# Kernel tuning notes

Measured on AMD Instinct MI355X. Metric: run time of the kernel, lower is better.

## Reference

```python
import jax, jax.numpy as jnp
import numpy as np

B, T, C = 4, 2048, 1024
N_HEAD = 16
HS = C // N_HEAD  # head_size = 64


def setup_inputs() -> dict:
    key = jax.random.key(0)
    k1, k2, k3 = jax.random.split(key, 3)
    x = jax.random.normal(k1, (B, T, C), dtype=jnp.float32)
    # torch Linear(in, out, bias=False); stored here as (in, out) so y = x @ W
    W_attn = jax.random.normal(k2, (C, 3 * C), dtype=jnp.float32) * (C ** -0.5)
    W_proj = jax.random.normal(k3, (C, C), dtype=jnp.float32) * (C ** -0.5)
    return {"x": x, "W_attn": W_attn, "W_proj": W_proj}


def reference(x, W_attn, W_proj):
    Bq, Tq, Cq = x.shape
    qkv = x @ W_attn                              # (B, T, 3C)
    q, k, v = jnp.split(qkv, 3, axis=-1)          # each (B, T, C)
    # (B, T, C) -> (B, H, T, hs)
    q = q.reshape(Bq, Tq, N_HEAD, HS).transpose(0, 2, 1, 3)
    k = k.reshape(Bq, Tq, N_HEAD, HS).transpose(0, 2, 1, 3)
    v = v.reshape(Bq, Tq, N_HEAD, HS).transpose(0, 2, 1, 3)
    scale = HS ** -0.5
    att = jnp.einsum("bhqd,bhkd->bhqk", q, k) * scale  # (B, H, T, T)
    causal = jnp.tril(jnp.ones((Tq, Tq), dtype=bool))
    att = jnp.where(causal[None, None], att, jnp.finfo(att.dtype).min)
    att = jax.nn.softmax(att, axis=-1)
    y = jnp.einsum("bhqk,bhkd->bhqd", att, v)     # (B, H, T, hs)
    y = y.transpose(0, 2, 1, 3).reshape(Bq, Tq, Cq)
    return y @ W_proj                             # (B, T, C)
```

## Files before the change

### kernel.cpp

```cpp
#include <hip/hip_runtime.h>
#include <stdint.h>

typedef __bf16 bf16x8 __attribute__((ext_vector_type(8)));
typedef float f32x4 __attribute__((ext_vector_type(4)));

__device__ __forceinline__ unsigned short f2bf(float f) {
  unsigned u = __builtin_bit_cast(unsigned, f);
  u = (u + 0x7fffu + ((u >> 16) & 1u)) >> 16;
  return (unsigned short)u;
}

__device__ __forceinline__ unsigned cvt_pk_bf16(float a, float b) {
  unsigned r;
  asm("v_cvt_pk_bf16_f32 %0, %1, %2" : "=v"(r) : "v"(a), "v"(b));
  return r;
}

__device__ __forceinline__ void gload_lds16(const unsigned short* g, unsigned short* l) {
  __builtin_amdgcn_global_load_lds(
      (__attribute__((address_space(1))) unsigned int*)g,
      (__attribute__((address_space(3))) unsigned int*)l, 16, 0, 0);
}

__device__ __forceinline__ void store_val(float* p, float v) { *p = v; }
__device__ __forceinline__ void store_val(unsigned short* p, float v) { *p = f2bf(v); }

__global__ __launch_bounds__(256) void f2bf_kernel(const float* __restrict__ in,
                                                   unsigned short* __restrict__ out, int n) {
  int stride = gridDim.x * blockDim.x * 4;
  for (int i = (blockIdx.x * blockDim.x + threadIdx.x) * 4; i < n; i += stride) {
    float4 v = *(const float4*)(in + i);
    ushort4 o;
    o.x = f2bf(v.x); o.y = f2bf(v.y); o.z = f2bf(v.z); o.w = f2bf(v.w);
    *(ushort4*)(out + i) = o;
  }
}

__global__ __launch_bounds__(256) void transpose_f2bf(const float* __restrict__ in,
                                                      unsigned short* __restrict__ out,
                                                      int R, int Ccols) {
  __shared__ unsigned short t[64][65];
  int r0 = blockIdx.y * 64, c0 = blockIdx.x * 64;
  int tid = threadIdx.x;
#pragma unroll
  for (int rep = 0; rep < 16; rep++) {
    int idx = rep * 256 + tid;
    int rr = idx >> 6, cc = idx & 63;
    t[rr][cc] = f2bf(in[(size_t)(r0 + rr) * Ccols + c0 + cc]);
  }
  __syncthreads();
#pragma unroll
  for (int rep = 0; rep < 16; rep++) {
    int idx = rep * 256 + tid;
    int cc = idx >> 6, rr = idx & 63;
    out[(size_t)(c0 + cc) * R + r0 + rr] = t[rr][cc];
  }
}

__global__ __launch_bounds__(256) void make_vt(const unsigned short* __restrict__ qkv,
                                               unsigned short* __restrict__ vt) {
  __shared__ unsigned short t[64][65];
  int bh = blockIdx.x;
  int b = bh >> 4, h = bh & 15;
  int t0 = blockIdx.y * 64;
  int tid = threadIdx.x;
#pragma unroll
  for (int rep = 0; rep < 16; rep++) {
    int idx = rep * 256 + tid;
    int tt = idx >> 6, dd = idx & 63;
    t[tt][dd] = qkv[(size_t)(b * 2048 + t0 + tt) * 3072 + 2048 + h * 64 + dd];
  }
  __syncthreads();
#pragma unroll
  for (int rep = 0; rep < 16; rep++) {
    int idx = rep * 256 + tid;
    int dd = idx >> 6, tt = idx & 63;
    vt[(size_t)bh * 131072 + (size_t)dd * 2048 + t0 + tt] = t[tt][dd];
  }
}

template <typename OutT>
__global__ __launch_bounds__(256) void gemm_bt(const unsigned short* __restrict__ A,
                                               const unsigned short* __restrict__ Bt,
                                               OutT* __restrict__ C, int M, int N, int K) {
  __shared__ unsigned short a_lds[128 * 32];
  __shared__ unsigned short b_lds[128 * 32];
  int tid = threadIdx.x;
  int w = tid >> 6, l = tid & 63;
  int wr = w >> 1, wc = w & 1;
  int lr = l & 15, lg = l >> 4;
  int m0 = blockIdx.y * 128, n0 = blockIdx.x * 128;

  int r = tid >> 2;
  int scol = ((tid & 3) ^ (r & 3)) * 8;
  const unsigned short* gA = A + (size_t)(m0 + r) * K + scol;
  const unsigned short* gA2 = gA + (size_t)64 * K;
  const unsigned short* gB = Bt + (size_t)(n0 + r) * K + scol;
  const unsigned short* gB2 = gB + (size_t)64 * K;
  unsigned short* la = &a_lds[w * 512];
  unsigned short* la2 = &a_lds[2048 + w * 512];
  unsigned short* lb = &b_lds[w * 512];
  unsigned short* lb2 = &b_lds[2048 + w * 512];

  int xoff = (lg ^ (lr & 3)) * 8;

  f32x4 acc[4][4] = {};

  for (int k0 = 0; k0 < K; k0 += 32) {
    gload_lds16(gA + k0, la);
    gload_lds16(gA2 + k0, la2);
    gload_lds16(gB + k0, lb);
    gload_lds16(gB2 + k0, lb2);
    __syncthreads();
    bf16x8 af[4], bfr[4];
#pragma unroll
    for (int m = 0; m < 4; m++)
      af[m] = *(const bf16x8*)&a_lds[(wr * 64 + m * 16 + lr) * 32 + xoff];
#pragma unroll
    for (int n = 0; n < 4; n++)
      bfr[n] = *(const bf16x8*)&b_lds[(wc * 64 + n * 16 + lr) * 32 + xoff];
#pragma unroll
    for (int m = 0; m < 4; m++)
#pragma unroll
      for (int n = 0; n < 4; n++)
        acc[m][n] = __builtin_amdgcn_mfma_f32_16x16x32_bf16(af[m], bfr[n], acc[m][n], 0, 0, 0);
    __syncthreads();
  }

#pragma unroll
  for (int m = 0; m < 4; m++)
#pragma unroll
    for (int n = 0; n < 4; n++)
#pragma unroll
      for (int i = 0; i < 4; i++) {
        size_t row = (size_t)(m0 + wr * 64 + m * 16 + lg * 4 + i);
        size_t col = (size_t)(n0 + wc * 64 + n * 16 + lr);
        store_val(&C[row * N + col], acc[m][n][i]);
      }
}

__global__ __launch_bounds__(256, 2) void attn_kernel(const unsigned short* __restrict__ qkv,
                                                      const unsigned short* __restrict__ vt,
                                                      unsigned short* __restrict__ y) {
  __shared__ unsigned short k_lds[2][64 * 64];
  __shared__ unsigned short v_lds[2][64 * 64];
  __shared__ unsigned short p_lds[8][16 * 64];
  int tid = threadIdx.x;
  int w = tid >> 6, l = tid & 63;
  int lr = l & 15, lg = l >> 4;
  int g4 = lg * 4;
  int lband = l & 48;
  int bh = blockIdx.x;
  int b = bh >> 4, h = bh & 15;
  int qgrp = 15 - blockIdx.y;
  int q0 = qgrp * 128 + w * 32;

  char* plo = (char*)p_lds[w * 2];
  char* phi = (char*)p_lds[w * 2 + 1];

  int srow = tid >> 3;
  int schunk = (tid & 7) ^ (srow & 7);
  const unsigned short* gK0 = qkv + (size_t)(b * 2048 + srow) * 3072 + 1024 + h * 64 + schunk * 8;
  const unsigned short* gK1 = gK0 + (size_t)32 * 3072;
  const unsigned short* gV0 = vt + (size_t)bh * 131072 + (size_t)srow * 2048 + schunk * 8;
  const unsigned short* gV1 = gV0 + (size_t)32 * 2048;
  int ldsbase0 = w * 512;
  int ldsbase1 = 2048 + w * 512;

  const unsigned short* qp = qkv + (size_t)(b * 2048 + q0 + lr) * 3072 + h * 64 + lg * 8;
  bf16x8 aQ0lo = *(const bf16x8*)qp;
  bf16x8 aQ1lo = *(const bf16x8*)(qp + 32);
  bf16x8 aQ0hi = *(const bf16x8*)(qp + 16 * 3072);
  bf16x8 aQ1hi = *(const bf16x8*)(qp + 16 * 3072 + 32);

  f32x4 Olo[4] = {}, Ohi[4] = {};
  float mlo = -3.0e38f, mhi = -3.0e38f;
  float sumlo = 0.f, sumhi = 0.f;
  const float SC = 0.125f * 1.44269504f;

  int rx = lr & 7;
  int kc0 = (lg ^ rx) * 8;
  int kc1 = ((4 + lg) ^ rx) * 8;

  int nbmax = ((qgrp * 128 + 96) >> 6) + 1;
  int kend = q0 + 31;
  int kdiag = q0 >> 6;

  gload_lds16(gK0, &k_lds[0][ldsbase0]);
  gload_lds16(gK1, &k_lds[0][ldsbase1]);
  gload_lds16(gV0, &v_lds[0][ldsbase0]);
  gload_lds16(gV1, &v_lds[0][ldsbase1]);
  __syncthreads();

  int cur = 0;
  for (int kb = 0; kb < nbmax; kb++) {
    int kbase = kb * 64;
    if (kb + 1 < nbmax) {
      size_t koff = (size_t)(kbase + 64) * 3072;
      size_t voff = (size_t)(kbase + 64);
      int nxt = cur ^ 1;
      gload_lds16(gK0 + koff, &k_lds[nxt][ldsbase0]);
      gload_lds16(gK1 + koff, &k_lds[nxt][ldsbase1]);
      gload_lds16(gV0 + voff, &v_lds[nxt][ldsbase0]);
      gload_lds16(gV1 + voff, &v_lds[nxt][ldsbase1]);
    }
    if (kbase <= kend) {
      const unsigned short* kl = k_lds[cur];
      const unsigned short* vl = v_lds[cur];
      f32x4 svlo[4], svhi[4];
      __builtin_amdgcn_s_setprio(1);
#pragma unroll
      for (int n = 0; n < 4; n++) {
        bf16x8 kf0 = *(const bf16x8*)&kl[(n * 16 + lr) * 64 + kc0];
        bf16x8 kf1 = *(const bf16x8*)&kl[(n * 16 + lr) * 64 + kc1];
        f32x4 z = {};
        z = __builtin_amdgcn_mfma_f32_16x16x32_bf16(kf0, aQ0lo, z, 0, 0, 0);
        z = __builtin_amdgcn_mfma_f32_16x16x32_bf16(kf1, aQ1lo, z, 0, 0, 0);
        svlo[n] = z;
        f32x4 z2 = {};
        z2 = __builtin_amdgcn_mfma_f32_16x16x32_bf16(kf0, aQ0hi, z2, 0, 0, 0);
        z2 = __builtin_amdgcn_mfma_f32_16x16x32_bf16(kf1, aQ1hi, z2, 0, 0, 0);
        svhi[n] = z2;
      }
      __builtin_amdgcn_s_setprio(0);
      float slo[4][4], shi[4][4];
#pragma unroll
      for (int n = 0; n < 4; n++)
#pragma unroll
        for (int i = 0; i < 4; i++) {
          slo[n][i] = svlo[n][i] * SC;
          shi[n][i] = svhi[n][i] * SC;
        }
      if (kb == kdiag) {
#pragma unroll
        for (int n = 0; n < 4; n++)
#pragma unroll
          for (int i = 0; i < 4; i++) {
            int kk = kbase + n * 16 + g4 + i;
            if (kk > q0 + lr) slo[n][i] = -1.0e38f;
            if (kk > q0 + 16 + lr) shi[n][i] = -1.0e38f;
          }
      }
      float tmlo = fmaxf(
          fmaxf(fmaxf(fmaxf(slo[0][0], slo[0][1]), fmaxf(slo[0][2], slo[0][3])),
                fmaxf(fmaxf(slo[1][0], slo[1][1]), fmaxf(slo[1][2], slo[1][3]))),
          fmaxf(fmaxf(fmaxf(slo[2][0], slo[2][1]), fmaxf(slo[2][2], slo[2][3])),
                fmaxf(fmaxf(slo[3][0], slo[3][1]), fmaxf(slo[3][2], slo[3][3]))));
      float tmhi = fmaxf(
          fmaxf(fmaxf(fmaxf(shi[0][0], shi[0][1]), fmaxf(shi[0][2], shi[0][3])),
                fmaxf(fmaxf(shi[1][0], shi[1][1]), fmaxf(shi[1][2], shi[1][3]))),
          fmaxf(fmaxf(fmaxf(shi[2][0], shi[2][1]), fmaxf(shi[2][2], shi[2][3])),
                fmaxf(fmaxf(shi[3][0], shi[3][1]), fmaxf(shi[3][2], shi[3][3]))));
      tmlo = fmaxf(tmlo, __shfl_xor(tmlo, 16));
      tmlo = fmaxf(tmlo, __shfl_xor(tmlo, 32));
      tmhi = fmaxf(tmhi, __shfl_xor(tmhi, 16));
      tmhi = fmaxf(tmhi, __shfl_xor(tmhi, 32));
      if (__any(tmlo > mlo + 11.54f || tmhi > mhi + 11.54f)) {
        float mnlo = fmaxf(mlo, tmlo), mnhi = fmaxf(mhi, tmhi);
        float faclo = __builtin_amdgcn_exp2f(mlo - mnlo);
        float fachi = __builtin_amdgcn_exp2f(mhi - mnhi);
        mlo = mnlo; mhi = mnhi;
        sumlo *= faclo; sumhi *= fachi;
        float f0 = __shfl(faclo, lband | g4);
        float f1 = __shfl(faclo, lband | (g4 + 1));
        float f2 = __shfl(faclo, lband | (g4 + 2));
        float f3 = __shfl(faclo, lband | (g4 + 3));
        float h0 = __shfl(fachi, lband | g4);
        float h1 = __shfl(fachi, lband | (g4 + 1));
        float h2 = __shfl(fachi, lband | (g4 + 2));
        float h3 = __shfl(fachi, lband | (g4 + 3));
#pragma unroll
        for (int n2 = 0; n2 < 4; n2++) {
          Olo[n2][0] *= f0; Olo[n2][1] *= f1; Olo[n2][2] *= f2; Olo[n2][3] *= f3;
          Ohi[n2][0] *= h0; Ohi[n2][1] *= h1; Ohi[n2][2] *= h2; Ohi[n2][3] *= h3;
        }
      }
      float pslo = 0.f, pshi = 0.f;
      unsigned pk0lo[4], pk1lo[4], pk0hi[4], pk1hi[4];
#pragma unroll
      for (int n = 0; n < 4; n++) {
        float a0 = __builtin_amdgcn_exp2f(slo[n][0] - mlo);
        float a1 = __builtin_amdgcn_exp2f(slo[n][1] - mlo);
        float a2 = __builtin_amdgcn_exp2f(slo[n][2] - mlo);
        float a3 = __builtin_amdgcn_exp2f(slo[n][3] - mlo);
        pslo += (a0 + a1) + (a2 + a3);
        pk0lo[n] = cvt_pk_bf16(a0, a1);
        pk1lo[n] = cvt_pk_bf16(a2, a3);
        float c0 = __builtin_amdgcn_exp2f(shi[n][0] - mhi);
        float c1 = __builtin_amdgcn_exp2f(shi[n][1] - mhi);
        float c2 = __builtin_amdgcn_exp2f(shi[n][2] - mhi);
        float c3 = __builtin_amdgcn_exp2f(shi[n][3] - mhi);
        pshi += (c0 + c1) + (c2 + c3);
        pk0hi[n] = cvt_pk_bf16(c0, c1);
        pk1hi[n] = cvt_pk_bf16(c2, c3);
      }
      pslo += __shfl_xor(pslo, 16);
      pslo += __shfl_xor(pslo, 32);
      pshi += __shfl_xor(pshi, 16);
      pshi += __shfl_xor(pshi, 32);
      sumlo += pslo;
      sumhi += pshi;
#pragma unroll
      for (int n = 0; n < 4; n++) {
        int chunk = (2 * n + (lg >> 1)) ^ (lr & 7);
        int off = lr * 128 + chunk * 16 + (lg & 1) * 8;
        *(uint2*)(plo + off) = make_uint2(pk0lo[n], pk1lo[n]);
        *(uint2*)(phi + off) = make_uint2(pk0hi[n], pk1hi[n]);
      }
      bf16x8 aPlo0 = *(const bf16x8*)(plo + lr * 128 + (lg ^ rx) * 16);
      bf16x8 aPlo1 = *(const bf16x8*)(plo + lr * 128 + ((4 + lg) ^ rx) * 16);
      bf16x8 aPhi0 = *(const bf16x8*)(phi + lr * 128 + (lg ^ rx) * 16);
      bf16x8 aPhi1 = *(const bf16x8*)(phi + lr * 128 + ((4 + lg) ^ rx) * 16);
      __builtin_amdgcn_s_setprio(1);
#pragma unroll
      for (int n2 = 0; n2 < 4; n2++) {
        bf16x8 v0 = *(const bf16x8*)&vl[(n2 * 16 + lr) * 64 + kc0];
        bf16x8 v1 = *(const bf16x8*)&vl[(n2 * 16 + lr) * 64 + kc1];
        Olo[n2] = __builtin_amdgcn_mfma_f32_16x16x32_bf16(aPlo0, v0, Olo[n2], 0, 0, 0);
        Olo[n2] = __builtin_amdgcn_mfma_f32_16x16x32_bf16(aPlo1, v1, Olo[n2], 0, 0, 0);
        Ohi[n2] = __builtin_amdgcn_mfma_f32_16x16x32_bf16(aPhi0, v0, Ohi[n2], 0, 0, 0);
        Ohi[n2] = __builtin_amdgcn_mfma_f32_16x16x32_bf16(aPhi1, v1, Ohi[n2], 0, 0, 0);
      }
      __builtin_amdgcn_s_setprio(0);
    }
    __syncthreads();
    cur ^= 1;
  }
  float s0 = __shfl(sumlo, lband | g4);
  float s1 = __shfl(sumlo, lband | (g4 + 1));
  float s2 = __shfl(sumlo, lband | (g4 + 2));
  float s3 = __shfl(sumlo, lband | (g4 + 3));
  float t0 = __shfl(sumhi, lband | g4);
  float t1 = __shfl(sumhi, lband | (g4 + 1));
  float t2 = __shfl(sumhi, lband | (g4 + 2));
  float t3 = __shfl(sumhi, lband | (g4 + 3));
  float rl0 = 1.f / s0, rl1 = 1.f / s1, rl2 = 1.f / s2, rl3 = 1.f / s3;
  float rh0 = 1.f / t0, rh1 = 1.f / t1, rh2 = 1.f / t2, rh3 = 1.f / t3;
#pragma unroll
  for (int n2 = 0; n2 < 4; n2++) {
    size_t base = (size_t)(b * 2048 + q0 + g4) * 1024 + h * 64 + n2 * 16 + lr;
    y[base] = f2bf(Olo[n2][0] * rl0);
    y[base + 1024] = f2bf(Olo[n2][1] * rl1);
    y[base + 2048] = f2bf(Olo[n2][2] * rl2);
    y[base + 3072] = f2bf(Olo[n2][3] * rl3);
    size_t bhh = base + (size_t)16 * 1024;
    y[bhh] = f2bf(Ohi[n2][0] * rh0);
    y[bhh + 1024] = f2bf(Ohi[n2][1] * rh1);
    y[bhh + 2048] = f2bf(Ohi[n2][2] * rh2);
    y[bhh + 3072] = f2bf(Ohi[n2][3] * rh3);
  }
}

extern "C" void kernel_launch(void* const* d_in, const int* in_sizes, int n_in,
                              void* d_out, int out_size, void* d_ws, size_t ws_size,
                              hipStream_t stream) {
  const float* x = (const float*)d_in[0];
  const float* Wa = (const float*)d_in[1];
  const float* Wp = (const float*)d_in[2];
  float* out = (float*)d_out;

  char* ws = (char*)d_ws;
  size_t off = 0;
  unsigned short* xb = (unsigned short*)(ws + off);   off += (size_t)8192 * 1024 * 2;
  unsigned short* Wta = (unsigned short*)(ws + off);  off += (size_t)3072 * 1024 * 2;
  unsigned short* Wtp = (unsigned short*)(ws + off);  off += (size_t)1024 * 1024 * 2;
  unsigned short* qkvb = (unsigned short*)(ws + off); off += (size_t)8192 * 3072 * 2;
  unsigned short* vtb = (unsigned short*)(ws + off);  off += (size_t)64 * 64 * 2048 * 2;
  unsigned short* yb = (unsigned short*)(ws + off);   off += (size_t)8192 * 1024 * 2;

  f2bf_kernel<<<2048, 256, 0, stream>>>(x, xb, 8192 * 1024);
  transpose_f2bf<<<dim3(48, 16), 256, 0, stream>>>(Wa, Wta, 1024, 3072);
  transpose_f2bf<<<dim3(16, 16), 256, 0, stream>>>(Wp, Wtp, 1024, 1024);
  gemm_bt<unsigned short><<<dim3(24, 64), 256, 0, stream>>>(xb, Wta, qkvb, 8192, 3072, 1024);
  make_vt<<<dim3(64, 32), 256, 0, stream>>>(qkvb, vtb);
  attn_kernel<<<dim3(64, 16), 256, 0, stream>>>(qkvb, vtb, yb);
  gemm_bt<float><<<dim3(8, 64), 256, 0, stream>>>(yb, Wtp, out, 8192, 1024, 1024);
}
```

Before: 191.3 us.

## Rewrite bf16 GEMM with 128x256 tiles, triple-buffered LDS and XCD-aware block mapping

The GEMM kernel moves from 128x128 tiles with K-step 32 and synchronous single buffering to 128x256 tiles with K-step 64, 512 threads, and a three-stage LDS ring. Global-to-LDS loads for stage t+2 are interleaved with MFMA work on stage t, and explicit vmcnt waits replace the paired syncthreads. Blocks are remapped with a modulo-8 swizzle to spread tiles across XCDs, and s_setprio raises wave priority around the MFMA bursts. The aim is to hide memory latency and improve data reuse in both projection GEMMs. The cost is about 144KB of LDS per block, which limits occupancy, plus more fragile hand-written wait counts.

```diff
diff --git a/kernel.cpp b/kernel.cpp
--- a/kernel.cpp
+++ b/kernel.cpp
@@ -80,61 +80,128 @@
 }
 
 template <typename OutT>
-__global__ __launch_bounds__(256) void gemm_bt(const unsigned short* __restrict__ A,
-                                               const unsigned short* __restrict__ Bt,
-                                               OutT* __restrict__ C, int M, int N, int K) {
-  __shared__ unsigned short a_lds[128 * 32];
-  __shared__ unsigned short b_lds[128 * 32];
-  int tid = threadIdx.x;
-  int w = tid >> 6, l = tid & 63;
-  int wr = w >> 1, wc = w & 1;
-  int lr = l & 15, lg = l >> 4;
-  int m0 = blockIdx.y * 128, n0 = blockIdx.x * 128;
-
-  int r = tid >> 2;
-  int scol = ((tid & 3) ^ (r & 3)) * 8;
-  const unsigned short* gA = A + (size_t)(m0 + r) * K + scol;
-  const unsigned short* gA2 = gA + (size_t)64 * K;
-  const unsigned short* gB = Bt + (size_t)(n0 + r) * K + scol;
-  const unsigned short* gB2 = gB + (size_t)64 * K;
-  unsigned short* la = &a_lds[w * 512];
-  unsigned short* la2 = &a_lds[2048 + w * 512];
-  unsigned short* lb = &b_lds[w * 512];
-  unsigned short* lb2 = &b_lds[2048 + w * 512];
-
-  int xoff = (lg ^ (lr & 3)) * 8;
+__global__ __launch_bounds__(512, 2) void gemm_bt(const unsigned short* __restrict__ A,
+                                                  const unsigned short* __restrict__ Bt,
+                                                  OutT* __restrict__ C, int M, int N, int K,
+                                                  int mtiles) {
+  __shared__ unsigned short lds3[3][24576];
+  const int tid = threadIdx.x;
+  const int wid = tid >> 6, l = tid & 63;
+  const int wm = wid >> 2, wn = wid & 3;
+  const int lr = l & 15, lg = l >> 4;
+
+  int nwg = gridDim.x;
+  int q8 = nwg >> 3;
+  int bid = blockIdx.x;
+  int bs = (bid & 7) * q8 + (bid >> 3);
+  int mt = bs % mtiles, nt = bs / mtiles;
+  const int m0 = mt * 128, n0 = nt * 256;
+
+  const int srow = tid >> 3;
+  const int schunk = ((tid & 7) ^ (srow & 7)) * 8;
+  const unsigned short* gA0 = A + (size_t)(m0 + srow) * K + schunk;
+  const unsigned short* gB0 = Bt + (size_t)(n0 + srow) * K + schunk;
+  const int wslice = wid * 512;
+
+  int arow[4], brow[2][2], xoff[2];
+#pragma unroll
+  for (int m = 0; m < 4; m++) arow[m] = (wm * 64 + m * 16 + lr) * 64;
+#pragma unroll
+  for (int qq = 0; qq < 2; qq++)
+#pragma unroll
+    for (int j = 0; j < 2; j++) brow[qq][j] = 8192 + (wn * 64 + qq * 32 + j * 16 + lr) * 64;
+#pragma unroll
+  for (int ks = 0; ks < 2; ks++) xoff[ks] = ((ks * 4 + lg) ^ (lr & 7)) * 8;
 
   f32x4 acc[4][4] = {};
-
-  for (int k0 = 0; k0 < K; k0 += 32) {
-    gload_lds16(gA + k0, la);
-    gload_lds16(gA2 + k0, la2);
-    gload_lds16(gB + k0, lb);
-    gload_lds16(gB2 + k0, lb2);
-    __syncthreads();
-    bf16x8 af[4], bfr[4];
+  const int NT = K >> 6;
+
+  gload_lds16(gA0, &lds3[0][wslice]);
+  gload_lds16(gA0 + (size_t)64 * K, &lds3[0][4096 + wslice]);
+#pragma unroll
+  for (int u = 0; u < 4; u++)
+    gload_lds16(gB0 + (size_t)(u * 64) * K, &lds3[0][8192 + u * 4096 + wslice]);
+  gload_lds16(gA0 + 64, &lds3[1][wslice]);
+  gload_lds16(gA0 + (size_t)64 * K + 64, &lds3[1][4096 + wslice]);
+#pragma unroll
+  for (int u = 0; u < 4; u++)
+    gload_lds16(gB0 + (size_t)(u * 64) * K + 64, &lds3[1][8192 + u * 4096 + wslice]);
+
+  int cb = 0;
+  for (int t = 0; t < NT; t++) {
+    if (t == NT - 1) {
+      asm volatile("s_waitcnt vmcnt(0)" ::: "memory");
+    } else {
+      asm volatile("s_waitcnt vmcnt(6)" ::: "memory");
+    }
+    __builtin_amdgcn_s_barrier();
+    const unsigned short* bufc = lds3[cb];
+    int pb = cb + 2; if (pb >= 3) pb -= 3;
+    unsigned short* bufp = lds3[pb];
+    const int k2 = (t + 2) * 64;
+    const bool pre = (t + 2) < NT;
+
+    if (pre) {
+      gload_lds16(gA0 + k2, bufp + wslice);
+      gload_lds16(gA0 + (size_t)64 * K + k2, bufp + 4096 + wslice);
+      gload_lds16(gB0 + k2, bufp + 8192 + wslice);
+    }
+    bf16x8 af[4][2];
 #pragma unroll
     for (int m = 0; m < 4; m++)
-      af[m] = *(const bf16x8*)&a_lds[(wr * 64 + m * 16 + lr) * 32 + xoff];
+#pragma unroll
+      for (int ks = 0; ks < 2; ks++)
+        af[m][ks] = *(const bf16x8*)&bufc[arow[m] + xoff[ks]];
+    {
+      bf16x8 bq[2][2];
+#pragma unroll
+      for (int j = 0; j < 2; j++)
+#pragma unroll
+        for (int ks = 0; ks < 2; ks++)
+          bq[j][ks] = *(const bf16x8*)&bufc[brow[0][j] + xoff[ks]];
+      __builtin_amdgcn_s_setprio(1);
+#pragma unroll
+      for (int m = 0; m < 4; m++)
+#pragma unroll
+        for (int j = 0; j < 2; j++)
+#pragma unroll
+          for (int ks = 0; ks < 2; ks++)
+            acc[m][j] = __builtin_amdgcn_mfma_f32_16x16x32_bf16(af[m][ks], bq[j][ks], acc[m][j], 0, 0, 0);
+      __builtin_amdgcn_s_setprio(0);
+    }
+    if (pre) {
+      gload_lds16(gB0 + (size_t)64 * K + k2, bufp + 12288 + wslice);
+      gload_lds16(gB0 + (size_t)128 * K + k2, bufp + 16384 + wslice);
+      gload_lds16(gB0 + (size_t)192 * K + k2, bufp + 20480 + wslice);
+    }
+    {
+      bf16x8 bq[2][2];
+#pragma unroll
+      for (int j = 0; j < 2; j++)
+#pragma unroll
+        for (int ks = 0; ks < 2; ks++)
+          bq[j][ks] = *(const bf16x8*)&bufc[brow[1][j] + xoff[ks]];
+      __builtin_amdgcn_s_setprio(1);
+#pragma unroll
+      for (int m = 0; m < 4; m++)
+#pragma unroll
+        for (int j = 0; j < 2; j++)
+#pragma unroll
+          for (int ks = 0; ks < 2; ks++)
+            acc[m][2 + j] = __builtin_amdgcn_mfma_f32_16x16x32_bf16(af[m][ks], bq[j][ks], acc[m][2 + j], 0, 0, 0);
+      __builtin_amdgcn_s_setprio(0);
+    }
+    cb = (cb == 2) ? 0 : cb + 1;
+  }
+
+#pragma unroll
+  for (int m = 0; m < 4; m++)
 #pragma unroll
     for (int n = 0; n < 4; n++)
-      bfr[n] = *(const bf16x8*)&b_lds[(wc * 64 + n * 16 + lr) * 32 + xoff];
-#pragma unroll
-    for (int m = 0; m < 4; m++)
-#pragma unroll
-      for (int n = 0; n < 4; n++)
-        acc[m][n] = __builtin_amdgcn_mfma_f32_16x16x32_bf16(af[m], bfr[n], acc[m][n], 0, 0, 0);
-    __syncthreads();
-  }
-
-#pragma unroll
-  for (int m = 0; m < 4; m++)
-#pragma unroll
-    for (int n = 0; n < 4; n++)
 #pragma unroll
       for (int i = 0; i < 4; i++) {
-        size_t row = (size_t)(m0 + wr * 64 + m * 16 + lg * 4 + i);
-        size_t col = (size_t)(n0 + wc * 64 + n * 16 + lr);
+        size_t row = (size_t)(m0 + wm * 64 + m * 16 + lg * 4 + i);
+        size_t col = (size_t)(n0 + wn * 64 + n * 16 + lr);
         store_val(&C[row * N + col], acc[m][n][i]);
       }
 }
@@ -371,8 +438,8 @@
   f2bf_kernel<<<2048, 256, 0, stream>>>(x, xb, 8192 * 1024);
   transpose_f2bf<<<dim3(48, 16), 256, 0, stream>>>(Wa, Wta, 1024, 3072);
   transpose_f2bf<<<dim3(16, 16), 256, 0, stream>>>(Wp, Wtp, 1024, 1024);
-  gemm_bt<unsigned short><<<dim3(24, 64), 256, 0, stream>>>(xb, Wta, qkvb, 8192, 3072, 1024);
+  gemm_bt<unsigned short><<<768, 512, 0, stream>>>(xb, Wta, qkvb, 8192, 3072, 1024, 64);
   make_vt<<<dim3(64, 32), 256, 0, stream>>>(qkvb, vtb);
   attn_kernel<<<dim3(64, 16), 256, 0, stream>>>(qkvb, vtb, yb);
-  gemm_bt<float><<<dim3(8, 64), 256, 0, stream>>>(yb, Wtp, out, 8192, 1024, 1024);
-}
+  gemm_bt<float><<<256, 512, 0, stream>>>(yb, Wtp, out, 8192, 1024, 1024, 64);
+}
```

After: 174.8 us. 1.09x faster.
